# Performance work log

Hardware: AMD Instinct MI355X
Metric: run time of the kernel (lower is better)

The kernel has to match this reference:

```python
import jax, jax.numpy as jnp
import numpy as np

N = 65536      # flattened tokens
K = 8192       # codebook_size
D = 64         # codebook_dim
DECAY = 0.9
EPS = 1e-05


def setup_inputs() -> dict:
    key = jax.random.key(0)
    k1, k2, k3, k4 = jax.random.split(key, 4)
    z = jax.random.normal(k1, (N, D), dtype=jnp.float32)
    # codebook initialized uniform(-1, 1) in the torch module
    weight = jax.random.uniform(k2, (K, D), dtype=jnp.float32, minval=-1.0, maxval=1.0)
    # EMA state: positive cluster sizes, embed_avg near the codebook
    cluster_size = jax.random.uniform(k3, (K,), dtype=jnp.float32)
    embed_avg = weight + 0.01 * jax.random.normal(k4, (K, D), dtype=jnp.float32)
    return {"z": z, "weight": weight, "cluster_size": cluster_size, "embed_avg": embed_avg}


def reference(z, weight, cluster_size, embed_avg):
    # VectorQuantizer.ema_update: distances -> argmin -> gather -> EMA stats -> weight refresh
    zd = jax.lax.stop_gradient(z)  # torch uses z.detach() for distance/quant_error
    # distance[n,k] = ||z_n||^2 + ||c_k||^2 - 2 z_n . c_k   (addmm pattern)
    dist = (zd * zd).sum(1, keepdims=True) + (weight * weight).sum(1) - 2.0 * (zd @ weight.T)  # [N, K]
    token = jnp.argmin(dist, axis=1)                      # [N]
    embed = weight[token]                                  # gather [N, D]
    quant_error = jnp.mean(((embed - zd) ** 2).sum(1))

    # onehot_probs.sum(0) == per-code counts; onehot.T @ z == segment sum of z
    counts = jax.ops.segment_sum(jnp.ones((zd.shape[0],), zd.dtype), token, num_segments=K)  # [K]
    embed_sum = jax.ops.segment_sum(z, token, num_segments=K)                                # [K, D]

    new_cluster_size = cluster_size * DECAY + (1.0 - DECAY) * counts
    new_embed_avg = embed_avg * DECAY + (1.0 - DECAY) * embed_sum

    # ema_weight_update with num_tokens = codebook_size
    n = new_cluster_size.sum()
    smoothed = (new_cluster_size + EPS) / (n + K * EPS) * n
    new_weight = new_embed_avg / smoothed[:, None]

    return quant_error, new_weight, new_cluster_size, new_embed_avg
```

## Files before the change

kernel.cpp:

```cpp
#include <hip/hip_runtime.h>
#include <type_traits>

#define N_TOK 65536
#define K_CODE 8192
#define D_DIM 64

constexpr float DECAY = 0.9f;
constexpr float OMD = 0.1f;
constexpr float EPS = 1e-5f;

constexpr int OUT_QE = 0;
constexpr int OUT_W  = 1;
constexpr int OUT_CS = 1 + K_CODE * D_DIM;
constexpr int OUT_EA = OUT_CS + K_CODE;

constexpr int WS_QE     = 0;
constexpr int WS_NSUM   = 16;
constexpr int WS_COUNTS = 16 + 8 * 32;
constexpr int WS_EMBSUM = WS_COUNTS + K_CODE;
constexpr int WS_WHI    = WS_EMBSUM + K_CODE * D_DIM;
constexpr int WS_WLO    = WS_WHI + K_CODE * D_DIM / 2;
constexpr int WS_CNF    = WS_WLO + K_CODE * D_DIM / 2;

typedef __attribute__((ext_vector_type(16))) float floatx16;
typedef __attribute__((ext_vector_type(8)))  short short8;
typedef __attribute__((ext_vector_type(8)))  __bf16 bf16x8;

template <typename T, typename = void> struct mfma_takes : std::false_type {};
template <typename T>
struct mfma_takes<T, std::void_t<decltype(__builtin_amdgcn_mfma_f32_32x32x16_bf16(
    std::declval<T>(), std::declval<T>(), std::declval<floatx16>(), 0, 0, 0))>>
    : std::true_type {};

__device__ __forceinline__ floatx16 MFMA(short8 a, short8 b, floatx16 c) {
  if constexpr (mfma_takes<bf16x8>::value) {
    return __builtin_amdgcn_mfma_f32_32x32x16_bf16(
        __builtin_bit_cast(bf16x8, a), __builtin_bit_cast(bf16x8, b), c, 0, 0, 0);
  } else {
    return __builtin_amdgcn_mfma_f32_32x32x16_bf16(a, b, c, 0, 0, 0);
  }
}

__device__ __forceinline__ unsigned short bf16rne(float x) {
  unsigned int u = __float_as_uint(x);
  return (unsigned short)((u + 0x7FFFu + ((u >> 16) & 1u)) >> 16);
}

__device__ __forceinline__ void gload_lds16(const unsigned short* g, unsigned short* l) {
#if defined(__has_builtin) && __has_builtin(__builtin_amdgcn_global_load_lds)
  typedef __attribute__((address_space(1))) void gvoid;
  typedef __attribute__((address_space(3))) void lvoid;
  __builtin_amdgcn_global_load_lds((gvoid*)g, (lvoid*)l, 16, 0, 0);
#else
  *(uint4*)l = *(const uint4*)g;
#endif
}

__global__ void vq_prep(const float* __restrict__ w, const float* __restrict__ cs,
                        float* __restrict__ ws) {
  const int tid = threadIdx.x;
  const int gid = blockIdx.x * 256 + tid;
  ws[WS_EMBSUM + gid] = 0.0f;
  if (gid < K_CODE) ws[WS_COUNTS + gid] = 0.0f;

  const int d = tid & 63;
  const int kw = tid >> 6;
  const int k = blockIdx.x * 4 + kw;
  const float v = w[(size_t)k * D_DIM + d];
  const unsigned short h = bf16rne(v);
  const float hf = __uint_as_float((unsigned int)h << 16);
  const unsigned short l = bf16rne(v - hf);
  unsigned short* whi = (unsigned short*)(ws + WS_WHI);
  unsigned short* wlo = (unsigned short*)(ws + WS_WLO);
  const int pos = k * D_DIM + (((d >> 3) ^ (k & 7)) * 8) + (d & 7);
  whi[pos] = h;
  wlo[pos] = l;
  float s = v * v;
#pragma unroll
  for (int m = 32; m >= 1; m >>= 1) s += __shfl_xor(s, m);
  __shared__ float csp[4];
  if (d == 0) {
    (ws + WS_CNF)[k] = s + 64.0f;
    csp[kw] = cs[k];
  }
  __syncthreads();
  if (tid == 0) {
    atomicAdd(ws + WS_NSUM + ((blockIdx.x & 7) << 5),
              DECAY * (csp[0] + csp[1] + csp[2] + csp[3]));
  }
}

__global__ __launch_bounds__(512, 2) void vq_argmin(
    const float* __restrict__ z, float* __restrict__ ws)
{
  __shared__ __align__(16) unsigned short Wbuf[2][4][2][32 * 64];
  __shared__ float mind_s[2][256];
  __shared__ int   tok_s[2][256];

  const int tid  = threadIdx.x;
  const int w    = tid >> 6;
  const int lane = tid & 63;
  const int m    = lane & 31;
  const int h    = lane >> 5;
  const int tgp  = w & 3;
  const int hw   = w >> 2;
  const int tb   = blockIdx.x * 256;

  const unsigned short* whi = (const unsigned short*)(ws + WS_WHI);
  const unsigned short* wlo = (const unsigned short*)(ws + WS_WLO);
  const float*          cnf = ws + WS_CNF;

  short8 ah_a[4], al_a[4], ah_b[4], al_b[4];
  float znorm_a = 0.f, znorm_b = 0.f;
  auto loadA = [&](int sub, short8* AH, short8* AL, float& zn) {
    const float* zrow =
        z + (size_t)(tb + tgp * 64 + sub * 32 + m) * D_DIM + 8 * h;
#pragma unroll
    for (int s4 = 0; s4 < 4; ++s4) {
      const float4 v0 = *(const float4*)(zrow + 16 * s4);
      const float4 v1 = *(const float4*)(zrow + 16 * s4 + 4);
      const float vals[8] = {v0.x, v0.y, v0.z, v0.w, v1.x, v1.y, v1.z, v1.w};
#pragma unroll
      for (int j = 0; j < 8; ++j) {
        const float x = vals[j];
        zn += x * x;
        const float y = -2.0f * x;
        const unsigned short hb = bf16rne(y);
        const float hf = __uint_as_float((unsigned int)hb << 16);
        const unsigned short lb = bf16rne(y - hf);
        AH[s4][j] = (short)hb;
        AL[s4][j] = (short)lb;
      }
    }
    zn += __shfl_xor(zn, 32);
  };
  loadA(0, ah_a, al_a, znorm_a);
  loadA(1, ah_b, al_b, znorm_b);

  float kmin0[16], kmin1[16];
#pragma unroll
  for (int r = 0; r < 16; ++r) { kmin0[r] = 3.4e38f; kmin1[r] = 3.4e38f; }

  auto issueStage = [&](int sIdx, int bufIdx) {
#pragma unroll
    for (int i = 0; i < 2; ++i) {
      const int t = w * 2 + i;
      const int half = t >> 3, plane = (t >> 2) & 1, seg = t & 3;
      const unsigned short* src = (plane ? wlo : whi)
          + ((size_t)half * 4096 + (size_t)sIdx * 32) * D_DIM + seg * 512 + lane * 8;
      unsigned short* dst = &Wbuf[half][bufIdx][plane][seg * 512];
      gload_lds16(src, dst);
    }
  };

  int xoff[4];
#pragma unroll
  for (int s4 = 0; s4 < 4; ++s4) xoff[s4] = ((2 * s4 + h) ^ (m & 7)) * 8;
  const int mrow = m * 64;
  const int cbase = hw * 4096;

#define LOADBH(BH, BUF) do {                                          \
    const unsigned short* _p = &Wbuf[hw][(BUF)][0][mrow];             \
    BH[0] = *(const short8*)(_p + xoff[0]);                           \
    BH[1] = *(const short8*)(_p + xoff[1]);                           \
    BH[2] = *(const short8*)(_p + xoff[2]);                           \
    BH[3] = *(const short8*)(_p + xoff[3]);                           \
  } while (0)

#define LOADBL(BL, BUF) do {                                          \
    const unsigned short* _p = &Wbuf[hw][(BUF)][1][mrow];             \
    BL[0] = *(const short8*)(_p + xoff[0]);                           \
    BL[1] = *(const short8*)(_p + xoff[1]);                           \
    BL[2] = *(const short8*)(_p + xoff[2]);                           \
    BL[3] = *(const short8*)(_p + xoff[3]);                           \
  } while (0)

  issueStage(0, 0);
  issueStage(1, 1);
  float cn_cur = cnf[cbase + m];
  asm volatile("s_waitcnt vmcnt(0)" ::: "memory");
  __builtin_amdgcn_s_barrier();
  asm volatile("" ::: "memory");

  short8 bh[4], bl[4];
  LOADBH(bh, 0);

  for (int s = 0; s < 128; ++s) {
    issueStage((s + 2) & 127, (s + 2) & 3);
    const float cn_next = cnf[cbase + ((s + 1) & 127) * 32 + m];
    asm volatile("s_waitcnt vmcnt(3)" ::: "memory");
    __builtin_amdgcn_s_barrier();
    asm volatile("" ::: "memory");

    LOADBL(bl, s & 3);

    floatx16 acc0, acc1;
#pragma unroll
    for (int r = 0; r < 16; ++r) { acc0[r] = cn_cur; acc1[r] = cn_cur; }

    __builtin_amdgcn_s_setprio(1);
    acc0 = MFMA(ah_a[0], bh[0], acc0); acc1 = MFMA(ah_b[0], bh[0], acc1);
    acc0 = MFMA(ah_a[1], bh[1], acc0); acc1 = MFMA(ah_b[1], bh[1], acc1);
    acc0 = MFMA(ah_a[2], bh[2], acc0); acc1 = MFMA(ah_b[2], bh[2], acc1);
    acc0 = MFMA(ah_a[3], bh[3], acc0); acc1 = MFMA(ah_b[3], bh[3], acc1);
    acc0 = MFMA(al_a[0], bh[0], acc0); acc1 = MFMA(al_b[0], bh[0], acc1);
    acc0 = MFMA(al_a[1], bh[1], acc0); acc1 = MFMA(al_b[1], bh[1], acc1);
    acc0 = MFMA(al_a[2], bh[2], acc0); acc1 = MFMA(al_b[2], bh[2], acc1);
    acc0 = MFMA(al_a[3], bh[3], acc0); acc1 = MFMA(al_b[3], bh[3], acc1);
    __builtin_amdgcn_s_setprio(0);

    LOADBH(bh, (s + 1) & 3);
    __builtin_amdgcn_s_setprio(1);
    acc0 = MFMA(ah_a[0], bl[0], acc0); acc1 = MFMA(ah_b[0], bl[0], acc1);
    acc0 = MFMA(ah_a[1], bl[1], acc0); acc1 = MFMA(ah_b[1], bl[1], acc1);
    acc0 = MFMA(ah_a[2], bl[2], acc0); acc1 = MFMA(ah_b[2], bl[2], acc1);
    acc0 = MFMA(ah_a[3], bl[3], acc0); acc1 = MFMA(ah_b[3], bl[3], acc1);
    __builtin_amdgcn_s_setprio(0);

#pragma unroll
    for (int r = 0; r < 16; ++r) {
      kmin0[r] = fminf(kmin0[r],
          __uint_as_float((__float_as_uint(acc0[r]) & 0xFFFFFF00u) | (unsigned)s));
      kmin1[r] = fminf(kmin1[r],
          __uint_as_float((__float_as_uint(acc1[r]) & 0xFFFFFF00u) | (unsigned)s));
    }
    cn_cur = cn_next;
  }
#undef LOADBH
#undef LOADBL

#define REDUCE_WRITE(KM, SUB, ZN) do {                                      \
    _Pragma("unroll")                                                       \
    for (int r = 0; r < 16; ++r) {                                          \
      float kv = KM[r];                                                     \
      int mo = m;                                                           \
      _Pragma("unroll")                                                     \
      for (int mm = 1; mm < 32; mm <<= 1) {                                 \
        const float ov = __shfl_xor(kv, mm);                                \
        const int   om = __shfl_xor(mo, mm);                                \
        if (ov < kv || (ov == kv && om < mo)) { kv = ov; mo = om; }         \
      }                                                                     \
      const int mr = (r & 3) + 8 * (r >> 2) + 4 * h;                        \
      if (m == mr) {                                                        \
        const unsigned int kb = __float_as_uint(kv);                        \
        const int trow = tgp * 64 + (SUB) * 32 + mr;                        \
        tok_s[hw][trow] = hw * 4096 + (int)(kb & 0xFFu) * 32 + mo;          \
        mind_s[hw][trow] = __uint_as_float(kb & 0xFFFFFF00u) - 64.0f + (ZN);\
      }                                                                     \
    }                                                                       \
  } while (0)

  REDUCE_WRITE(kmin0, 0, znorm_a);
  REDUCE_WRITE(kmin1, 1, znorm_b);
#undef REDUCE_WRITE
  __syncthreads();

  float* counts = ws + WS_COUNTS;
  float* embsum = ws + WS_EMBSUM;

  if (tid < 256) {
    const float d0 = mind_s[0][tid], d1 = mind_s[1][tid];
    const int   i0 = tok_s[0][tid],  i1 = tok_s[1][tid];
    const bool t1 = d1 < d0;
    const float dm = t1 ? d1 : d0;
    const int   im = t1 ? i1 : i0;
    tok_s[0][tid] = im;
    float qe = dm;
#pragma unroll
    for (int mm = 32; mm >= 1; mm >>= 1) qe += __shfl_xor(qe, mm);
    if ((tid & 63) == 0) atomicAdd(ws + WS_QE, qe);
    atomicAdd(&counts[im], 1.0f);
  }
  __syncthreads();

#pragma unroll 4
  for (int t = 0; t < 32; ++t) {
    const int row = w * 32 + t;
    const int tk = tok_s[0][row];
    const float zv = z[(size_t)(tb + row) * D_DIM + lane];
    atomicAdd(&embsum[(size_t)tk * D_DIM + lane], zv);
  }
}

__global__ void vq_finalize(const float* __restrict__ cluster_size,
                            const float* __restrict__ embed_avg,
                            const float* __restrict__ ws, float* __restrict__ out)
{
  const int idx = blockIdx.x * 256 + threadIdx.x;
  const int k = idx >> 6;
  const float ncs = cluster_size[k] * DECAY + OMD * ws[WS_COUNTS + k];
  const float nea = embed_avg[idx] * DECAY + OMD * ws[WS_EMBSUM + idx];
  out[OUT_EA + idx] = nea;
  float n = OMD * (float)N_TOK;
#pragma unroll
  for (int i = 0; i < 8; ++i) n += ws[WS_NSUM + (i << 5)];
  const float sm = (ncs + EPS) / (n + K_CODE * EPS) * n;
  out[OUT_W + idx] = nea / sm;
  if ((idx & 63) == 0) out[OUT_CS + k] = ncs;
  if (idx == 0) out[OUT_QE] = ws[WS_QE] * (1.0f / N_TOK);
}

extern "C" void kernel_launch(void* const* d_in, const int* in_sizes, int n_in,
                              void* d_out, int out_size, void* d_ws, size_t ws_size,
                              hipStream_t stream) {
  const float* z  = (const float*)d_in[0];
  const float* w  = (const float*)d_in[1];
  const float* cs = (const float*)d_in[2];
  const float* ea = (const float*)d_in[3];
  float* out = (float*)d_out;
  float* ws  = (float*)d_ws;

  (void)hipMemsetAsync(d_ws, 0, (size_t)WS_COUNTS * sizeof(float), stream);

  vq_prep<<<K_CODE / 4, 256, 0, stream>>>(w, cs, ws);
  vq_argmin<<<N_TOK / 256, 512, 0, stream>>>(z, ws);
  vq_finalize<<<K_CODE * D_DIM / 256, 256, 0, stream>>>(cs, ea, ws, out);
}
```

Before: 279.0 us.

## Halve argmin block size and split MFMA accumulation into independent chains

The argmin kernel now runs 256-thread blocks covering 128 tokens each, doubling the grid. Each wave issues four codebook-stage loads instead of two, and the waitcnt is adjusted to match. Inside the loop, the hi-plane and lo-plane products now go into separate accumulators that are summed before the min update, which shortens dependent MFMA chains. In exchange, each codebook tile is streamed by twice as many blocks, and there are fewer waves per block to hide latency.

```diff
diff --git a/kernel.cpp b/kernel.cpp
--- a/kernel.cpp
+++ b/kernel.cpp
@@ -90,21 +90,21 @@
   }
 }
 
-__global__ __launch_bounds__(512, 2) void vq_argmin(
+__global__ __launch_bounds__(256, 2) void vq_argmin(
     const float* __restrict__ z, float* __restrict__ ws)
 {
   __shared__ __align__(16) unsigned short Wbuf[2][4][2][32 * 64];
-  __shared__ float mind_s[2][256];
-  __shared__ int   tok_s[2][256];
+  __shared__ float mind_s[2][128];
+  __shared__ int   tok_s[2][128];
 
   const int tid  = threadIdx.x;
   const int w    = tid >> 6;
   const int lane = tid & 63;
   const int m    = lane & 31;
   const int h    = lane >> 5;
-  const int tgp  = w & 3;
-  const int hw   = w >> 2;
-  const int tb   = blockIdx.x * 256;
+  const int tgp  = w & 1;
+  const int hw   = w >> 1;
+  const int tb   = blockIdx.x * 128;
 
   const unsigned short* whi = (const unsigned short*)(ws + WS_WHI);
   const unsigned short* wlo = (const unsigned short*)(ws + WS_WLO);
@@ -143,8 +143,8 @@
 
   auto issueStage = [&](int sIdx, int bufIdx) {
 #pragma unroll
-    for (int i = 0; i < 2; ++i) {
-      const int t = w * 2 + i;
+    for (int i = 0; i < 4; ++i) {
+      const int t = w * 4 + i;
       const int half = t >> 3, plane = (t >> 2) & 1, seg = t & 3;
       const unsigned short* src = (plane ? wlo : whi)
           + ((size_t)half * 4096 + (size_t)sIdx * 32) * D_DIM + seg * 512 + lane * 8;
@@ -184,45 +184,49 @@
 
   short8 bh[4], bl[4];
   LOADBH(bh, 0);
+  const floatx16 kZero = {};
 
   for (int s = 0; s < 128; ++s) {
     issueStage((s + 2) & 127, (s + 2) & 3);
     const float cn_next = cnf[cbase + ((s + 1) & 127) * 32 + m];
-    asm volatile("s_waitcnt vmcnt(3)" ::: "memory");
+    asm volatile("s_waitcnt vmcnt(5)" ::: "memory");
     __builtin_amdgcn_s_barrier();
     asm volatile("" ::: "memory");
 
     LOADBL(bl, s & 3);
 
-    floatx16 acc0, acc1;
-#pragma unroll
-    for (int r = 0; r < 16; ++r) { acc0[r] = cn_cur; acc1[r] = cn_cur; }
-
+    floatx16 cnv;
+#pragma unroll
+    for (int r = 0; r < 16; ++r) cnv[r] = cn_cur;
+
+    floatx16 A0, B0, A1, B1;
     __builtin_amdgcn_s_setprio(1);
-    acc0 = MFMA(ah_a[0], bh[0], acc0); acc1 = MFMA(ah_b[0], bh[0], acc1);
-    acc0 = MFMA(ah_a[1], bh[1], acc0); acc1 = MFMA(ah_b[1], bh[1], acc1);
-    acc0 = MFMA(ah_a[2], bh[2], acc0); acc1 = MFMA(ah_b[2], bh[2], acc1);
-    acc0 = MFMA(ah_a[3], bh[3], acc0); acc1 = MFMA(ah_b[3], bh[3], acc1);
-    acc0 = MFMA(al_a[0], bh[0], acc0); acc1 = MFMA(al_b[0], bh[0], acc1);
-    acc0 = MFMA(al_a[1], bh[1], acc0); acc1 = MFMA(al_b[1], bh[1], acc1);
-    acc0 = MFMA(al_a[2], bh[2], acc0); acc1 = MFMA(al_b[2], bh[2], acc1);
-    acc0 = MFMA(al_a[3], bh[3], acc0); acc1 = MFMA(al_b[3], bh[3], acc1);
+    A0 = MFMA(ah_a[0], bh[0], cnv);   A1 = MFMA(ah_b[0], bh[0], cnv);
+    B0 = MFMA(al_a[0], bh[0], kZero); B1 = MFMA(al_b[0], bh[0], kZero);
+    A0 = MFMA(ah_a[1], bh[1], A0);    A1 = MFMA(ah_b[1], bh[1], A1);
+    B0 = MFMA(al_a[1], bh[1], B0);    B1 = MFMA(al_b[1], bh[1], B1);
+    A0 = MFMA(ah_a[2], bh[2], A0);    A1 = MFMA(ah_b[2], bh[2], A1);
+    B0 = MFMA(al_a[2], bh[2], B0);    B1 = MFMA(al_b[2], bh[2], B1);
+    A0 = MFMA(ah_a[3], bh[3], A0);    A1 = MFMA(ah_b[3], bh[3], A1);
+    B0 = MFMA(al_a[3], bh[3], B0);    B1 = MFMA(al_b[3], bh[3], B1);
     __builtin_amdgcn_s_setprio(0);
 
     LOADBH(bh, (s + 1) & 3);
     __builtin_amdgcn_s_setprio(1);
-    acc0 = MFMA(ah_a[0], bl[0], acc0); acc1 = MFMA(ah_b[0], bl[0], acc1);
-    acc0 = MFMA(ah_a[1], bl[1], acc0); acc1 = MFMA(ah_b[1], bl[1], acc1);
-    acc0 = MFMA(ah_a[2], bl[2], acc0); acc1 = MFMA(ah_b[2], bl[2], acc1);
-    acc0 = MFMA(ah_a[3], bl[3], acc0); acc1 = MFMA(ah_b[3], bl[3], acc1);
+    A0 = MFMA(ah_a[0], bl[0], A0);    A1 = MFMA(ah_b[0], bl[0], A1);
+    B0 = MFMA(ah_a[2], bl[2], B0);    B1 = MFMA(ah_b[2], bl[2], B1);
+    A0 = MFMA(ah_a[1], bl[1], A0);    A1 = MFMA(ah_b[1], bl[1], A1);
+    B0 = MFMA(ah_a[3], bl[3], B0);    B1 = MFMA(ah_b[3], bl[3], B1);
     __builtin_amdgcn_s_setprio(0);
 
 #pragma unroll
     for (int r = 0; r < 16; ++r) {
+      const float v0 = A0[r] + B0[r];
+      const float v1 = A1[r] + B1[r];
       kmin0[r] = fminf(kmin0[r],
-          __uint_as_float((__float_as_uint(acc0[r]) & 0xFFFFFF00u) | (unsigned)s));
+          __uint_as_float((__float_as_uint(v0) & 0xFFFFFF00u) | (unsigned)s));
       kmin1[r] = fminf(kmin1[r],
-          __uint_as_float((__float_as_uint(acc1[r]) & 0xFFFFFF00u) | (unsigned)s));
+          __uint_as_float((__float_as_uint(v1) & 0xFFFFFF00u) | (unsigned)s));
     }
     cn_cur = cn_next;
   }
@@ -258,7 +262,7 @@
   float* counts = ws + WS_COUNTS;
   float* embsum = ws + WS_EMBSUM;
 
-  if (tid < 256) {
+  if (tid < 128) {
     const float d0 = mind_s[0][tid], d1 = mind_s[1][tid];
     const int   i0 = tok_s[0][tid],  i1 = tok_s[1][tid];
     const bool t1 = d1 < d0;
@@ -313,6 +317,6 @@
   (void)hipMemsetAsync(d_ws, 0, (size_t)WS_COUNTS * sizeof(float), stream);
 
   vq_prep<<<K_CODE / 4, 256, 0, stream>>>(w, cs, ws);
-  vq_argmin<<<N_TOK / 256, 512, 0, stream>>>(z, ws);
+  vq_argmin<<<N_TOK / 128, 256, 0, stream>>>(z, ws);
   vq_finalize<<<K_CODE * D_DIM / 256, 256, 0, stream>>>(cs, ea, ws, out);
 }
```

Measured after the change: 292.7 us. 1.05x slower.

## Split codebook across four wave groups with 1024-thread argmin blocks

Applied to the files above, without the earlier changes.

Doubles the argmin block to 1024 threads so four wave groups each scan a quarter of the codebook (2048 codes, 64 stages) instead of two groups each scanning half. The per-token partial minima are then reduced over four quarters in shared memory, and the embed-sum scatter loop is split over twice as many waves. This shortens the serial per-block loop and raises the number of waves per CU. In exchange it doubles LDS staging per block, which may cut how many blocks fit per CU, and the launch bound of 1024 threads at 4 blocks may force register spilling.

```diff
diff --git a/kernel.cpp b/kernel.cpp
--- a/kernel.cpp
+++ b/kernel.cpp
@@ -90,12 +90,12 @@
   }
 }
 
-__global__ __launch_bounds__(512, 2) void vq_argmin(
+__global__ __launch_bounds__(1024, 4) void vq_argmin(
     const float* __restrict__ z, float* __restrict__ ws)
 {
-  __shared__ __align__(16) unsigned short Wbuf[2][4][2][32 * 64];
-  __shared__ float mind_s[2][256];
-  __shared__ int   tok_s[2][256];
+  __shared__ __align__(16) unsigned short Wbuf[4][4][2][32 * 64];
+  __shared__ float mind_s[4][256];
+  __shared__ int   tok_s[4][256];
 
   const int tid  = threadIdx.x;
   const int w    = tid >> 6;
@@ -103,7 +103,7 @@
   const int m    = lane & 31;
   const int h    = lane >> 5;
   const int tgp  = w & 3;
-  const int hw   = w >> 2;
+  const int qw   = w >> 2;
   const int tb   = blockIdx.x * 256;
 
   const unsigned short* whi = (const unsigned short*)(ws + WS_WHI);
@@ -145,10 +145,10 @@
 #pragma unroll
     for (int i = 0; i < 2; ++i) {
       const int t = w * 2 + i;
-      const int half = t >> 3, plane = (t >> 2) & 1, seg = t & 3;
+      const int q = t >> 3, plane = (t >> 2) & 1, seg = t & 3;
       const unsigned short* src = (plane ? wlo : whi)
-          + ((size_t)half * 4096 + (size_t)sIdx * 32) * D_DIM + seg * 512 + lane * 8;
-      unsigned short* dst = &Wbuf[half][bufIdx][plane][seg * 512];
+          + ((size_t)q * 2048 + (size_t)sIdx * 32) * D_DIM + seg * 512 + lane * 8;
+      unsigned short* dst = &Wbuf[q][bufIdx][plane][seg * 512];
       gload_lds16(src, dst);
     }
   };
@@ -157,10 +157,10 @@
 #pragma unroll
   for (int s4 = 0; s4 < 4; ++s4) xoff[s4] = ((2 * s4 + h) ^ (m & 7)) * 8;
   const int mrow = m * 64;
-  const int cbase = hw * 4096;
+  const int cbase = qw * 2048;
 
 #define LOADBH(BH, BUF) do {                                          \
-    const unsigned short* _p = &Wbuf[hw][(BUF)][0][mrow];             \
+    const unsigned short* _p = &Wbuf[qw][(BUF)][0][mrow];             \
     BH[0] = *(const short8*)(_p + xoff[0]);                           \
     BH[1] = *(const short8*)(_p + xoff[1]);                           \
     BH[2] = *(const short8*)(_p + xoff[2]);                           \
@@ -168,7 +168,7 @@
   } while (0)
 
 #define LOADBL(BL, BUF) do {                                          \
-    const unsigned short* _p = &Wbuf[hw][(BUF)][1][mrow];             \
+    const unsigned short* _p = &Wbuf[qw][(BUF)][1][mrow];             \
     BL[0] = *(const short8*)(_p + xoff[0]);                           \
     BL[1] = *(const short8*)(_p + xoff[1]);                           \
     BL[2] = *(const short8*)(_p + xoff[2]);                           \
@@ -185,9 +185,9 @@
   short8 bh[4], bl[4];
   LOADBH(bh, 0);
 
-  for (int s = 0; s < 128; ++s) {
-    issueStage((s + 2) & 127, (s + 2) & 3);
-    const float cn_next = cnf[cbase + ((s + 1) & 127) * 32 + m];
+  for (int s = 0; s < 64; ++s) {
+    issueStage((s + 2) & 63, (s + 2) & 3);
+    const float cn_next = cnf[cbase + ((s + 1) & 63) * 32 + m];
     asm volatile("s_waitcnt vmcnt(3)" ::: "memory");
     __builtin_amdgcn_s_barrier();
     asm volatile("" ::: "memory");
@@ -244,8 +244,8 @@
       if (m == mr) {                                                        \
         const unsigned int kb = __float_as_uint(kv);                        \
         const int trow = tgp * 64 + (SUB) * 32 + mr;                        \
-        tok_s[hw][trow] = hw * 4096 + (int)(kb & 0xFFu) * 32 + mo;          \
-        mind_s[hw][trow] = __uint_as_float(kb & 0xFFFFFF00u) - 64.0f + (ZN);\
+        tok_s[qw][trow] = qw * 2048 + (int)(kb & 0xFFu) * 32 + mo;          \
+        mind_s[qw][trow] = __uint_as_float(kb & 0xFFFFFF00u) - 64.0f + (ZN);\
       }                                                                     \
     }                                                                       \
   } while (0)
@@ -259,11 +259,14 @@
   float* embsum = ws + WS_EMBSUM;
 
   if (tid < 256) {
-    const float d0 = mind_s[0][tid], d1 = mind_s[1][tid];
-    const int   i0 = tok_s[0][tid],  i1 = tok_s[1][tid];
-    const bool t1 = d1 < d0;
-    const float dm = t1 ? d1 : d0;
-    const int   im = t1 ? i1 : i0;
+    float dm = mind_s[0][tid];
+    int   im = tok_s[0][tid];
+#pragma unroll
+    for (int q = 1; q < 4; ++q) {
+      const float dq = mind_s[q][tid];
+      const int   iq = tok_s[q][tid];
+      if (dq < dm) { dm = dq; im = iq; }
+    }
     tok_s[0][tid] = im;
     float qe = dm;
 #pragma unroll
@@ -274,8 +277,8 @@
   __syncthreads();
 
 #pragma unroll 4
-  for (int t = 0; t < 32; ++t) {
-    const int row = w * 32 + t;
+  for (int t = 0; t < 16; ++t) {
+    const int row = w * 16 + t;
     const int tk = tok_s[0][row];
     const float zv = z[(size_t)(tb + row) * D_DIM + lane];
     atomicAdd(&embsum[(size_t)tk * D_DIM + lane], zv);
@@ -313,6 +316,6 @@
   (void)hipMemsetAsync(d_ws, 0, (size_t)WS_COUNTS * sizeof(float), stream);
 
   vq_prep<<<K_CODE / 4, 256, 0, stream>>>(w, cs, ws);
-  vq_argmin<<<N_TOK / 256, 512, 0, stream>>>(z, ws);
+  vq_argmin<<<N_TOK / 256, 1024, 0, stream>>>(z, ws);
   vq_finalize<<<K_CODE * D_DIM / 256, 256, 0, stream>>>(cs, ea, ws, out);
 }
```

New measurement: 930.2 us. 233% more time.
